# Kernel optimization log

Hardware: AMD Instinct MI355X
Metric: run time of the kernel (lower is better)

Reference implementation:

```python
import jax, jax.numpy as jnp
import numpy as np

B, L, HID = 2, 2048, 2048
NH, NKV, HD = 16, 4, 128
LAT = 512
Q_PER_KV = NH // NKV
SCALE = HD ** -0.5
ROPE_THETA = 10000.0


def setup_inputs() -> dict:
    key = jax.random.key(0)
    ks = jax.random.split(key, 6)
    s = lambda fan_in: 1.0 / np.sqrt(fan_in)
    return {
        "x": jax.random.normal(ks[0], (B, L, HID), dtype=jnp.float32),
        "Wq": jax.random.normal(ks[1], (HID, NH * HD), dtype=jnp.float32) * s(HID),
        "Wc": jax.random.normal(ks[2], (HID, LAT), dtype=jnp.float32) * s(HID),
        "Wk": jax.random.normal(ks[3], (LAT, NKV * HD), dtype=jnp.float32) * s(LAT),
        "Wv": jax.random.normal(ks[4], (LAT, NKV * HD), dtype=jnp.float32) * s(LAT),
        "Wo": jax.random.normal(ks[5], (NH * HD, HID), dtype=jnp.float32) * s(NH * HD),
        "attention_mask": jnp.ones((B, L), dtype=jnp.int32),
    }


def _rope(t):  # t: [B, H, L, HD]
    half = HD // 2
    inv_freq = 1.0 / (ROPE_THETA ** (jnp.arange(half, dtype=jnp.float32) / half))
    pos = jnp.arange(t.shape[2], dtype=jnp.float32)
    freqs = pos[:, None] * inv_freq[None, :]          # [L, half]
    cos = jnp.cos(freqs)[None, None].astype(t.dtype)  # [1,1,L,half]
    sin = jnp.sin(freqs)[None, None].astype(t.dtype)
    t1, t2 = t[..., :half], t[..., half:]
    return jnp.concatenate([t1 * cos - t2 * sin, t2 * cos + t1 * sin], axis=-1)


def reference(x, Wq, Wc, Wk, Wv, Wo, attention_mask):
    q = (x @ Wq).reshape(B, L, NH, HD).transpose(0, 2, 1, 3)      # [B,NH,L,HD]
    c = x @ Wc                                                    # latent bottleneck
    k = (c @ Wk).reshape(B, L, NKV, HD).transpose(0, 2, 1, 3)     # [B,NKV,L,HD]
    v = (c @ Wv).reshape(B, L, NKV, HD).transpose(0, 2, 1, 3)
    # GQA repeat_interleave along head axis
    k = jnp.repeat(k, Q_PER_KV, axis=1)                           # [B,NH,L,HD]
    v = jnp.repeat(v, Q_PER_KV, axis=1)
    q = _rope(q)
    k = _rope(k)
    att = jnp.einsum("bhqd,bhkd->bhqk", q, k) * SCALE             # [B,NH,L,L]
    neg = jnp.finfo(att.dtype).min
    causal = jnp.tril(jnp.ones((L, L), dtype=bool))[None, None]
    att = jnp.where(causal, att, neg)
    key_mask = (attention_mask > 0)[:, None, None, :]             # [B,1,1,L]
    att = jnp.where(key_mask, att, neg)
    att = jax.nn.softmax(att, axis=-1)
    y = jnp.einsum("bhqk,bhkd->bhqd", att, v)
    y = y.transpose(0, 2, 1, 3).reshape(B, L, NH * HD)
    return y @ Wo
```

## Files before the change

kernel.cpp:

```cpp
#include <hip/hip_runtime.h>
#include <hip/hip_bf16.h>
#include <cstdint>
#include <cstddef>

#define B_    2
#define L_    2048
#define HID_  2048
#define NH_   16
#define NKV_  4
#define HD_   128
#define LAT_  512
#define SCALE_ 0.08838834764831845f
#define SC2_   0.1275174365f

typedef unsigned short u16;
typedef unsigned int   u32;
typedef __attribute__((ext_vector_type(8))) short   short8;
typedef __attribute__((ext_vector_type(4))) float   floatx4;

typedef __attribute__((address_space(1))) const u32 gas_u32;
typedef __attribute__((address_space(3))) u32       las_u32;

__device__ __forceinline__ void gl_lds16(const u16* g, u16* l) {
    __builtin_amdgcn_global_load_lds((gas_u32*)g, (las_u32*)l, 16, 0, 0);
}

__device__ __forceinline__ float bf2f(u16 u) {
    union { u32 i; float f; } v; v.i = ((u32)u) << 16; return v.f;
}
__device__ __forceinline__ u16 f2bf(float f) {
    union { float f; u32 u; } v; v.f = f;
    u32 u = v.u;
    u32 r = (u + 0x7fffu + ((u >> 16) & 1u)) >> 16;
    return (u16)r;
}
__device__ __forceinline__ u16 f2bf_hw(float f) {
    union { __hip_bfloat16 h; u16 u; } c;
    c.h = __float2bfloat16(f);
    return c.u;
}

__global__ void cvt_kernel(const float* __restrict__ in, u16* __restrict__ out, int n4) {
    int i = blockIdx.x * 256 + threadIdx.x;
    if (i < n4) {
        float4 v = ((const float4*)in)[i];
        union { u16 w[4]; uint2 v; } o;
        o.w[0] = f2bf(v.x); o.w[1] = f2bf(v.y);
        o.w[2] = f2bf(v.z); o.w[3] = f2bf(v.w);
        ((uint2*)out)[i] = o.v;
    }
}

__global__ void cvt_transpose_kernel(const float* __restrict__ in, u16* __restrict__ out,
                                     int R, int C) {
    __shared__ u16 tile[32][33];
    int c0 = blockIdx.x * 32, r0 = blockIdx.y * 32;
    int tx = threadIdx.x & 31, ty = threadIdx.x >> 5;
    for (int i = ty; i < 32; i += 8)
        tile[tx][i] = f2bf(in[(size_t)(r0 + i) * C + c0 + tx]);
    __syncthreads();
    for (int i = ty; i < 32; i += 8)
        out[(size_t)(c0 + i) * R + r0 + tx] = tile[i][tx];
}

__global__ void transpose_v_kernel(const u16* __restrict__ in, u16* __restrict__ out) {
    __shared__ u16 t[32][33];
    int lt = blockIdx.x, dt = blockIdx.y, bh = blockIdx.z;
    int b = bh >> 2, kvh = bh & 3;
    int tx = threadIdx.x & 31, ty = threadIdx.x >> 5;
    for (int i = ty; i < 32; i += 8)
        t[i][tx] = in[(((size_t)b * L_ + lt * 32 + i) * NKV_ + kvh) * HD_ + dt * 32 + tx];
    __syncthreads();
    const int lcol = lt * 32 + tx;
    const int csig = (lcol & ~63) | ((lcol & 15) << 2) | ((lcol >> 4) & 3);
    for (int i = ty; i < 32; i += 8)
        out[((size_t)bh * HD_ + dt * 32 + i) * L_ + csig] = t[tx][i];
}

template<int OUT_BF16>
__global__ __launch_bounds__(256)
void gemm_bt(const u16* __restrict__ A, const u16* __restrict__ BT,
             void* __restrict__ C, int M, int N, int K) {
    __shared__ __align__(16) u16 As[128][32];
    __shared__ __align__(16) u16 Bs[128][32];
    const int tid  = threadIdx.x;
    const int m0   = blockIdx.y * 128, n0 = blockIdx.x * 128;
    const int wave = tid >> 6, lane = tid & 63;
    const int wm   = (wave >> 1) * 64, wn = (wave & 1) * 64;
    const int quad = lane >> 4, l16 = lane & 15;

    const int srow = wave * 32 + (lane >> 2);
    const int scol = (lane & 3) * 8;
    const u16* aptr0 = A  + (size_t)(m0 + srow) * K + scol;
    const u16* bptr0 = BT + (size_t)(n0 + srow) * K + scol;
    const u16* aptr1 = aptr0 + (size_t)16 * K;
    const u16* bptr1 = bptr0 + (size_t)16 * K;
    u16* lA0 = &As[wave * 32][0];
    u16* lA1 = &As[wave * 32 + 16][0];
    u16* lB0 = &Bs[wave * 32][0];
    u16* lB1 = &Bs[wave * 32 + 16][0];

    floatx4 acc[4][4] = {};

    for (int k0 = 0; k0 < K; k0 += 32) {
        gl_lds16(aptr0 + k0, lA0);
        gl_lds16(aptr1 + k0, lA1);
        gl_lds16(bptr0 + k0, lB0);
        gl_lds16(bptr1 + k0, lB1);
        __syncthreads();

        short8 af[4], bfr[4];
        #pragma unroll
        for (int i = 0; i < 4; i++) af[i]  = *(const short8*)&As[wm + i * 16 + l16][quad * 8];
        #pragma unroll
        for (int i = 0; i < 4; i++) bfr[i] = *(const short8*)&Bs[wn + i * 16 + l16][quad * 8];
        #pragma unroll
        for (int mi = 0; mi < 4; mi++)
            #pragma unroll
            for (int ni = 0; ni < 4; ni++)
                acc[mi][ni] = __builtin_amdgcn_mfma_f32_16x16x32_bf16(
                    af[mi], bfr[ni], acc[mi][ni], 0, 0, 0);
        __syncthreads();
    }

    #pragma unroll
    for (int mi = 0; mi < 4; mi++) {
        #pragma unroll
        for (int ni = 0; ni < 4; ni++) {
            #pragma unroll
            for (int r = 0; r < 4; r++) {
                int row = m0 + wm + mi * 16 + quad * 4 + r;
                int col = n0 + wn + ni * 16 + l16;
                float v = acc[mi][ni][r];
                if (OUT_BF16) ((u16*)C)[(size_t)row * N + col] = f2bf(v);
                else          ((float*)C)[(size_t)row * N + col] = v;
            }
        }
    }
}

__global__ __launch_bounds__(256)
void gemm_bt_split(const u16* __restrict__ A, const u16* __restrict__ BT,
                   u16* __restrict__ C0, u16* __restrict__ C1,
                   int M, int N, int K, int Nsplit, int N0, int N1) {
    __shared__ __align__(16) u16 As[128][32];
    __shared__ __align__(16) u16 Bs[128][32];
    const int tid  = threadIdx.x;
    const int m0   = blockIdx.y * 128, n0 = blockIdx.x * 128;
    const int wave = tid >> 6, lane = tid & 63;
    const int wm   = (wave >> 1) * 64, wn = (wave & 1) * 64;
    const int quad = lane >> 4, l16 = lane & 15;

    const int srow = wave * 32 + (lane >> 2);
    const int scol = (lane & 3) * 8;
    const u16* aptr0 = A  + (size_t)(m0 + srow) * K + scol;
    const u16* bptr0 = BT + (size_t)(n0 + srow) * K + scol;
    const u16* aptr1 = aptr0 + (size_t)16 * K;
    const u16* bptr1 = bptr0 + (size_t)16 * K;
    u16* lA0 = &As[wave * 32][0];
    u16* lA1 = &As[wave * 32 + 16][0];
    u16* lB0 = &Bs[wave * 32][0];
    u16* lB1 = &Bs[wave * 32 + 16][0];

    floatx4 acc[4][4] = {};

    for (int k0 = 0; k0 < K; k0 += 32) {
        gl_lds16(aptr0 + k0, lA0);
        gl_lds16(aptr1 + k0, lA1);
        gl_lds16(bptr0 + k0, lB0);
        gl_lds16(bptr1 + k0, lB1);
        __syncthreads();

        short8 af[4], bfr[4];
        #pragma unroll
        for (int i = 0; i < 4; i++) af[i]  = *(const short8*)&As[wm + i * 16 + l16][quad * 8];
        #pragma unroll
        for (int i = 0; i < 4; i++) bfr[i] = *(const short8*)&Bs[wn + i * 16 + l16][quad * 8];
        #pragma unroll
        for (int mi = 0; mi < 4; mi++)
            #pragma unroll
            for (int ni = 0; ni < 4; ni++)
                acc[mi][ni] = __builtin_amdgcn_mfma_f32_16x16x32_bf16(
                    af[mi], bfr[ni], acc[mi][ni], 0, 0, 0);
        __syncthreads();
    }

    const int side = (n0 >= Nsplit);
    u16* Cw = side ? C1 : C0;
    const int nw = side ? N1 : N0;
    const int cbase = side ? Nsplit : 0;

    #pragma unroll
    for (int mi = 0; mi < 4; mi++) {
        #pragma unroll
        for (int ni = 0; ni < 4; ni++) {
            #pragma unroll
            for (int r = 0; r < 4; r++) {
                int row = m0 + wm + mi * 16 + quad * 4 + r;
                int col = n0 + wn + ni * 16 + l16 - cbase;
                Cw[(size_t)row * nw + col] = f2bf(acc[mi][ni][r]);
            }
        }
    }
}

__global__ void rope_perm(const u16* __restrict__ in, u16* __restrict__ out,
                          int nh, int nhbits) {
    int idx = blockIdx.x * 256 + threadIdx.x;
    int d = idx & 63;
    int l = (idx >> 6) & (L_ - 1);
    int h = (idx >> 17) & (nh - 1);
    int b = idx >> (17 + nhbits);
    const u16* src = &in[(((size_t)b * L_ + l) * nh + h) * HD_];
    u16* dst = &out[(((size_t)b * nh + h) * L_ + l) * HD_];
    float t1 = bf2f(src[d]), t2 = bf2f(src[d + 64]);
    float inv = expf(-(float)d * 0.14391156831212787f);
    float fr = (float)l * inv;
    float c = cosf(fr), sn = sinf(fr);
    dst[d]      = f2bf(t1 * c - t2 * sn);
    dst[d + 64] = f2bf(t2 * c + t1 * sn);
}

__global__ __launch_bounds__(256)
void attn_mfma(const u16* __restrict__ Q, const u16* __restrict__ K,
               const u16* __restrict__ Vt, const int* __restrict__ amask,
               u16* __restrict__ Y, float* __restrict__ Opart,
               float* __restrict__ lpart) {
    __shared__ __align__(16) u16 Ks[64][128];
    __shared__ __align__(16) u16 Vs[128][64];
    __shared__ int smask[64];

    const int tid  = threadIdx.x;
    const int wave = tid >> 6, lane = tid & 63;
    const int quad = lane >> 4, l16 = lane & 15;

    const int bid = blockIdx.x;
    const int s   = bid >> 8;
    const int c   = bid & 255;
    const int bkvh = c & 7;
    const int j   = c >> 3;
    const int b   = bkvh >> 2, kvh = bkvh & 3;

    const int H  = ((32 + j) >> 1) + 1;
    const int Lg = ((31 - j) >> 1) + 1;
    const int m2 = max((H + 1) >> 1, (Lg + 1) >> 1);
    const int m3 = max((H + 2) / 3, Lg);
    const int nh = (m2 <= m3) ? 2 : 3;
    const int nl = 4 - nh;
    int t, kt0, kt1, pi;
    if (s < nh) {
        t = 32 + j; kt0 = (H * s) / nh; kt1 = (H * (s + 1)) / nh; pi = bid;
    } else {
        t = 31 - j;
        const int ls = s - nh;
        kt0 = (Lg * ls) / nl; kt1 = (Lg * (ls + 1)) / nl;
        pi = (nl == 1) ? -1 : bid;
    }

    const int h   = kvh * 4 + wave;
    const int q0  = t * 32;

    const u16* Qbase = Q  + ((size_t)b * NH_  + h)   * L_ * HD_;
    const u16* Kbase = K  + ((size_t)b * NKV_ + kvh) * L_ * HD_;
    const u16* Vbase = Vt + ((size_t)b * NKV_ + kvh) * (size_t)HD_ * L_;
    const int* mbase = amask + b * L_;

    short8 qa[2][4];
    #pragma unroll
    for (int mi = 0; mi < 2; ++mi)
        #pragma unroll
        for (int ks = 0; ks < 4; ++ks)
            qa[mi][ks] = *(const short8*)&Qbase[(size_t)(q0 + mi * 16 + l16) * HD_ + ks * 32 + quad * 8];

    floatx4 Oacc[2][8] = {};
    float lsum[2][4] = {};

    const int krow = tid >> 2, kq0 = (tid & 3) * 4;
    const int vrow = tid >> 1, vc0 = (tid & 1) * 4;
    const int kr7  = krow & 7, vr7 = vrow & 7;
    u16* kdst0 = &Ks[krow][((kq0 + 0) ^ kr7) * 8];
    u16* kdst1 = &Ks[krow][((kq0 + 1) ^ kr7) * 8];
    u16* kdst2 = &Ks[krow][((kq0 + 2) ^ kr7) * 8];
    u16* kdst3 = &Ks[krow][((kq0 + 3) ^ kr7) * 8];
    u16* vdst0 = &Vs[vrow][((vc0 + 0) ^ vr7) * 8];
    u16* vdst1 = &Vs[vrow][((vc0 + 1) ^ vr7) * 8];
    u16* vdst2 = &Vs[vrow][((vc0 + 2) ^ vr7) * 8];
    u16* vdst3 = &Vs[vrow][((vc0 + 3) ^ vr7) * 8];
    const u16* ksrc = Kbase + ((size_t)(kt0 * 64 + krow)) * HD_ + kq0 * 8;
    const u16* vsrc = Vbase + (size_t)vrow * L_ + kt0 * 64 + vc0 * 8;

    u16* Psb = &Ks[0][0] + wave * 2048;

    for (int kt = kt0; kt < kt1; ++kt) {
        const int kbase = kt * 64;

        *(uint4*)kdst0 = *(const uint4*)(ksrc);
        *(uint4*)kdst1 = *(const uint4*)(ksrc + 8);
        *(uint4*)kdst2 = *(const uint4*)(ksrc + 16);
        *(uint4*)kdst3 = *(const uint4*)(ksrc + 24);
        *(uint4*)vdst0 = *(const uint4*)(vsrc);
        *(uint4*)vdst1 = *(const uint4*)(vsrc + 8);
        *(uint4*)vdst2 = *(const uint4*)(vsrc + 16);
        *(uint4*)vdst3 = *(const uint4*)(vsrc + 24);
        if (tid < 64) smask[tid] = mbase[kbase + tid];
        ksrc += (size_t)64 * HD_;
        vsrc += 64;
        __syncthreads();

        floatx4 sfr[2][4] = {};
        __builtin_amdgcn_s_setprio(1);
        #pragma unroll
        for (int ni = 0; ni < 4; ++ni) {
            #pragma unroll
            for (int ks = 0; ks < 4; ++ks) {
                short8 kf = *(const short8*)&Ks[ni * 16 + l16][((ks * 4 + quad) ^ (l16 & 7)) * 8];
                sfr[0][ni] = __builtin_amdgcn_mfma_f32_16x16x32_bf16(qa[0][ks], kf, sfr[0][ni], 0, 0, 0);
                sfr[1][ni] = __builtin_amdgcn_mfma_f32_16x16x32_bf16(qa[1][ks], kf, sfr[1][ni], 0, 0, 0);
            }
        }
        __builtin_amdgcn_s_setprio(0);

        int am[4];
        #pragma unroll
        for (int ni = 0; ni < 4; ++ni) am[ni] = smask[ni * 16 + l16];

        __syncthreads();

        #pragma unroll
        for (int mi = 0; mi < 2; ++mi) {
            #pragma unroll
            for (int r = 0; r < 4; ++r) {
                const int qrow = q0 + mi * 16 + quad * 4 + r;
                union { u16 w[4]; uint2 v; } pb;
                #pragma unroll
                for (int ni = 0; ni < 4; ++ni) {
                    const int kpos = kbase + ni * 16 + l16;
                    const bool ok = (kpos <= qrow) & (am[ni] > 0);
                    float p = ok ? exp2f(fmaf(sfr[mi][ni][r], SC2_, -8.0f)) : 0.0f;
                    lsum[mi][r] += p;
                    pb.w[ni] = f2bf_hw(p);
                }
                const int row = mi * 16 + quad * 4 + r;
                *(uint2*)&Psb[row * 64 + ((l16 ^ ((row & 7) << 1)) << 2)] = pb.v;
            }
        }

        short8 pf[2][2];
        #pragma unroll
        for (int mi = 0; mi < 2; ++mi)
            #pragma unroll
            for (int kc = 0; kc < 2; ++kc) {
                const int row = mi * 16 + l16;
                const int p0 = (kc * 8 + quad * 2) ^ ((l16 & 7) << 1);
                pf[mi][kc] = *(const short8*)&Psb[row * 64 + p0 * 4];
            }

        __builtin_amdgcn_s_setprio(1);
        #pragma unroll
        for (int kc = 0; kc < 2; ++kc) {
            #pragma unroll
            for (int dn = 0; dn < 8; ++dn) {
                short8 vf = *(const short8*)&Vs[dn * 16 + l16][((kc * 4 + quad) ^ (l16 & 7)) * 8];
                Oacc[0][dn] = __builtin_amdgcn_mfma_f32_16x16x32_bf16(pf[0][kc], vf, Oacc[0][dn], 0, 0, 0);
                Oacc[1][dn] = __builtin_amdgcn_mfma_f32_16x16x32_bf16(pf[1][kc], vf, Oacc[1][dn], 0, 0, 0);
            }
        }
        __builtin_amdgcn_s_setprio(0);
        __syncthreads();
    }

    if (pi < 0) {
        #pragma unroll
        for (int mi = 0; mi < 2; ++mi) {
            #pragma unroll
            for (int r = 0; r < 4; ++r) {
                float v = lsum[mi][r];
                v += __shfl_xor(v, 1);
                v += __shfl_xor(v, 2);
                v += __shfl_xor(v, 4);
                v += __shfl_xor(v, 8);
                const float linv = 1.0f / v;
                const int qrow = q0 + mi * 16 + quad * 4 + r;
                u16* dst = &Y[(((size_t)b * L_ + qrow) * NH_ + h) * HD_];
                #pragma unroll
                for (int dn = 0; dn < 8; ++dn)
                    dst[dn * 16 + l16] = f2bf(Oacc[mi][dn][r] * linv);
            }
        }
    } else {
        float* od = Opart + ((size_t)pi * 4 + wave) * 32 * 128;
        float* lp = lpart + ((size_t)pi * 4 + wave) * 32;
        #pragma unroll
        for (int mi = 0; mi < 2; ++mi) {
            #pragma unroll
            for (int r = 0; r < 4; ++r) {
                float v = lsum[mi][r];
                v += __shfl_xor(v, 1);
                v += __shfl_xor(v, 2);
                v += __shfl_xor(v, 4);
                v += __shfl_xor(v, 8);
                const int qi = mi * 16 + quad * 4 + r;
                if (l16 == 0) __builtin_nontemporal_store(v, &lp[qi]);
                #pragma unroll
                for (int dn = 0; dn < 8; ++dn)
                    __builtin_nontemporal_store(Oacc[mi][dn][r],
                                                &od[(size_t)qi * 128 + dn * 16 + l16]);
            }
        }
    }
}

__global__ __launch_bounds__(256)
void attn_combine(const float* __restrict__ Opart, const float* __restrict__ lpart,
                  u16* __restrict__ Y) {
    const int cb = blockIdx.x;
    const int c  = cb & 255, z = cb >> 8;
    const int tile = z >> 2, hw = z & 3;
    const int bkvh = c & 7, j = c >> 3;
    const int b = bkvh >> 2, kvh = bkvh & 3;
    const int h = kvh * 4 + hw;
    const int H  = ((32 + j) >> 1) + 1;
    const int Lg = ((31 - j) >> 1) + 1;
    const int m2 = max((H + 1) >> 1, (Lg + 1) >> 1);
    const int m3 = max((H + 2) / 3, Lg);
    const int nh = (m2 <= m3) ? 2 : 3;
    const int nl = 4 - nh;
    if (tile == 1 && nl == 1) return;
    const int s0 = tile ? nh : 0;
    const int ns = tile ? nl : nh;
    const int t  = tile ? (31 - j) : (32 + j);
    const int tid = threadIdx.x;
    const int q = tid >> 3, dg = tid & 7;

    float4 a0 = {0,0,0,0}, a1 = {0,0,0,0}, a2 = {0,0,0,0}, a3 = {0,0,0,0};
    float lacc = 0.0f;
    for (int i = 0; i < ns; ++i) {
        const size_t rowb = ((size_t)((s0 + i) * 256 + c) * 4 + hw) * 32 + q;
        lacc += lpart[rowb];
        const float4* op = (const float4*)(Opart + rowb * 128 + dg * 16);
        float4 v0 = op[0], v1 = op[1], v2 = op[2], v3 = op[3];
        a0.x += v0.x; a0.y += v0.y; a0.z += v0.z; a0.w += v0.w;
        a1.x += v1.x; a1.y += v1.y; a1.z += v1.z; a1.w += v1.w;
        a2.x += v2.x; a2.y += v2.y; a2.z += v2.z; a2.w += v2.w;
        a3.x += v3.x; a3.y += v3.y; a3.z += v3.z; a3.w += v3.w;
    }
    const float linv = 1.0f / lacc;
    const int qrow = t * 32 + q;
    u16* dst = &Y[(((size_t)b * L_ + qrow) * NH_ + h) * HD_ + dg * 16];

    u16 tmp[16];
    tmp[0]  = f2bf(a0.x * linv); tmp[1]  = f2bf(a0.y * linv);
    tmp[2]  = f2bf(a0.z * linv); tmp[3]  = f2bf(a0.w * linv);
    tmp[4]  = f2bf(a1.x * linv); tmp[5]  = f2bf(a1.y * linv);
    tmp[6]  = f2bf(a1.z * linv); tmp[7]  = f2bf(a1.w * linv);
    tmp[8]  = f2bf(a2.x * linv); tmp[9]  = f2bf(a2.y * linv);
    tmp[10] = f2bf(a2.z * linv); tmp[11] = f2bf(a2.w * linv);
    tmp[12] = f2bf(a3.x * linv); tmp[13] = f2bf(a3.y * linv);
    tmp[14] = f2bf(a3.z * linv); tmp[15] = f2bf(a3.w * linv);
    *(uint4*)(dst)     = *(const uint4*)(&tmp[0]);
    *(uint4*)(dst + 8) = *(const uint4*)(&tmp[8]);
}

extern "C" void kernel_launch(void* const* d_in, const int* in_sizes, int n_in,
                              void* d_out, int out_size, void* d_ws, size_t ws_size,
                              hipStream_t stream) {
    const float* x  = (const float*)d_in[0];
    const float* Wq = (const float*)d_in[1];
    const float* Wc = (const float*)d_in[2];
    const float* Wk = (const float*)d_in[3];
    const float* Wv = (const float*)d_in[4];
    const float* Wo = (const float*)d_in[5];
    const int* amask = (const int*)d_in[6];
    float* out = (float*)d_out;

    char* p = (char*)d_ws;
    auto alloc = [&](size_t elems) {
        u16* r = (u16*)p;
        p += ((elems * 2 + 255) / 256) * 256;
        return r;
    };
    u16* WoT  = alloc((size_t)2048 * 2048);
    u16* qbuf = alloc((size_t)4096 * 2048);
    u16* Qr   = alloc((size_t)4096 * 2048);
    u16* Kr   = alloc((size_t)4096 * 512);
    u16* Vt   = alloc((size_t)4096 * 512);
    char* pdead = p;
    u16* Xb   = alloc((size_t)4096 * 2048);
    u16* WqT  = alloc((size_t)2048 * 2048);
    u16* WcT  = alloc((size_t)512 * 2048);
    u16* WkT  = alloc((size_t)512 * 512);
    u16* WvT  = alloc((size_t)512 * 512);
    u16* cbuf = alloc((size_t)4096 * 512);
    u16* kbuf = alloc((size_t)4096 * 512);
    u16* vbuf = alloc((size_t)4096 * 512);
    float* Opart = (float*)pdead;
    float* lpart = (float*)(pdead + (size_t)1024 * 4 * 32 * 128 * 4);

    cvt_kernel<<<8388608 / 4 / 256, 256, 0, stream>>>(x, Xb, 8388608 / 4);
    cvt_transpose_kernel<<<dim3(2048 / 32, 2048 / 32), 256, 0, stream>>>(Wq, WqT, 2048, 2048);
    cvt_transpose_kernel<<<dim3(512 / 32, 2048 / 32), 256, 0, stream>>>(Wc, WcT, 2048, 512);
    cvt_transpose_kernel<<<dim3(512 / 32, 512 / 32), 256, 0, stream>>>(Wk, WkT, 512, 512);
    cvt_transpose_kernel<<<dim3(512 / 32, 512 / 32), 256, 0, stream>>>(Wv, WvT, 512, 512);
    cvt_transpose_kernel<<<dim3(2048 / 32, 2048 / 32), 256, 0, stream>>>(Wo, WoT, 2048, 2048);

    gemm_bt_split<<<dim3(20, 32), 256, 0, stream>>>(Xb, WqT, qbuf, cbuf,
                                                    4096, 2560, 2048, 2048, 2048, 512);
    gemm_bt_split<<<dim3(8, 32), 256, 0, stream>>>(cbuf, WkT, kbuf, vbuf,
                                                   4096, 1024, 512, 512, 512, 512);

    rope_perm<<<(2 * 16 * 2048 * 64) / 256, 256, 0, stream>>>(qbuf, Qr, 16, 4);
    rope_perm<<<(2 * 4 * 2048 * 64) / 256, 256, 0, stream>>>(kbuf, Kr, 4, 2);
    transpose_v_kernel<<<dim3(64, 4, 8), 256, 0, stream>>>(vbuf, Vt);

    attn_mfma<<<dim3(1024), 256, 0, stream>>>(Qr, Kr, Vt, amask, qbuf, Opart, lpart);
    attn_combine<<<dim3(2048), 256, 0, stream>>>(Opart, lpart, qbuf);

    gemm_bt<0><<<dim3(16, 32), 256, 0, stream>>>(qbuf, WoT, out, 4096, 2048, 2048);
}
```

Before: 374.2 us.

## Keep attention probabilities in registers via transposed QK MFMA and direct LDS loads

The QK^T MFMA swaps its operands so each lane holds scores in the layout the PV MFMA needs. This removes the LDS round-trip for P and one __syncthreads per key tile, and the V transpose permutation is changed to match. K/V tiles are loaded with global_load_lds instead of register staging. A fast path skips masking when the tile is fully below the diagonal and the attention mask is all ones. Row sums are reduced with fewer shuffles. The risk is getting the layout permutation wrong and adding extra per-tile mask loads from global memory.

```diff
diff --git a/kernel.cpp b/kernel.cpp
--- a/kernel.cpp
+++ b/kernel.cpp
@@ -72,7 +72,10 @@
         t[i][tx] = in[(((size_t)b * L_ + lt * 32 + i) * NKV_ + kvh) * HD_ + dt * 32 + tx];
     __syncthreads();
     const int lcol = lt * 32 + tx;
-    const int csig = (lcol & ~63) | ((lcol & 15) << 2) | ((lcol >> 4) & 3);
+    const int k6 = lcol & 63;
+    const int ni = k6 >> 4, qd = (k6 >> 2) & 3, r = k6 & 3;
+    const int p = ((ni >> 1) << 5) | (qd << 3) | ((ni & 1) << 2) | r;
+    const int csig = (lcol & ~63) | p;
     for (int i = ty; i < 32; i += 8)
         out[((size_t)bh * HD_ + dt * 32 + i) * L_ + csig] = t[tx][i];
 }
@@ -228,7 +231,6 @@
                float* __restrict__ lpart) {
     __shared__ __align__(16) u16 Ks[64][128];
     __shared__ __align__(16) u16 Vs[128][64];
-    __shared__ int smask[64];
 
     const int tid  = threadIdx.x;
     const int wave = tid >> 6, lane = tid & 63;
@@ -273,38 +275,37 @@
             qa[mi][ks] = *(const short8*)&Qbase[(size_t)(q0 + mi * 16 + l16) * HD_ + ks * 32 + quad * 8];
 
     floatx4 Oacc[2][8] = {};
-    float lsum[2][4] = {};
-
-    const int krow = tid >> 2, kq0 = (tid & 3) * 4;
-    const int vrow = tid >> 1, vc0 = (tid & 1) * 4;
-    const int kr7  = krow & 7, vr7 = vrow & 7;
-    u16* kdst0 = &Ks[krow][((kq0 + 0) ^ kr7) * 8];
-    u16* kdst1 = &Ks[krow][((kq0 + 1) ^ kr7) * 8];
-    u16* kdst2 = &Ks[krow][((kq0 + 2) ^ kr7) * 8];
-    u16* kdst3 = &Ks[krow][((kq0 + 3) ^ kr7) * 8];
-    u16* vdst0 = &Vs[vrow][((vc0 + 0) ^ vr7) * 8];
-    u16* vdst1 = &Vs[vrow][((vc0 + 1) ^ vr7) * 8];
-    u16* vdst2 = &Vs[vrow][((vc0 + 2) ^ vr7) * 8];
-    u16* vdst3 = &Vs[vrow][((vc0 + 3) ^ vr7) * 8];
-    const u16* ksrc = Kbase + ((size_t)(kt0 * 64 + krow)) * HD_ + kq0 * 8;
-    const u16* vsrc = Vbase + (size_t)vrow * L_ + kt0 * 64 + vc0 * 8;
-
-    u16* Psb = &Ks[0][0] + wave * 2048;
+    float lsum[2] = {0.0f, 0.0f};
+
+    const int slK = lane & 15, rKl = lane >> 4;
+    const int slV = lane & 7,  rVl = lane >> 3;
+    int okg[4], ovg[4];
+    u16 *klds[4], *vlds[4];
+    #pragma unroll
+    for (int cc = 0; cc < 4; ++cc) {
+        const int seg = wave * 4 + cc;
+        const int rk = seg * 4 + rKl;
+        okg[cc] = rk * HD_ + ((slK ^ (rk & 7)) * 8);
+        klds[cc] = (u16*)Ks + seg * 512;
+        const int rv = seg * 8 + rVl;
+        ovg[cc] = rv * L_ + ((slV ^ (rv & 7)) * 8);
+        vlds[cc] = (u16*)Vs + seg * 512;
+    }
+    const u16* kgb = Kbase + (size_t)kt0 * 64 * HD_;
+    const u16* vgb = Vbase + kt0 * 64;
 
     for (int kt = kt0; kt < kt1; ++kt) {
         const int kbase = kt * 64;
 
-        *(uint4*)kdst0 = *(const uint4*)(ksrc);
-        *(uint4*)kdst1 = *(const uint4*)(ksrc + 8);
-        *(uint4*)kdst2 = *(const uint4*)(ksrc + 16);
-        *(uint4*)kdst3 = *(const uint4*)(ksrc + 24);
-        *(uint4*)vdst0 = *(const uint4*)(vsrc);
-        *(uint4*)vdst1 = *(const uint4*)(vsrc + 8);
-        *(uint4*)vdst2 = *(const uint4*)(vsrc + 16);
-        *(uint4*)vdst3 = *(const uint4*)(vsrc + 24);
-        if (tid < 64) smask[tid] = mbase[kbase + tid];
-        ksrc += (size_t)64 * HD_;
-        vsrc += 64;
+        #pragma unroll
+        for (int cc = 0; cc < 4; ++cc) {
+            gl_lds16(kgb + okg[cc], klds[cc]);
+            gl_lds16(vgb + ovg[cc], vlds[cc]);
+        }
+        const int am_l = mbase[kbase + lane];
+        const bool allm = __all(am_l > 0);
+        kgb += (size_t)64 * HD_;
+        vgb += 64;
         __syncthreads();
 
         floatx4 sfr[2][4] = {};
@@ -314,34 +315,40 @@
             #pragma unroll
             for (int ks = 0; ks < 4; ++ks) {
                 short8 kf = *(const short8*)&Ks[ni * 16 + l16][((ks * 4 + quad) ^ (l16 & 7)) * 8];
-                sfr[0][ni] = __builtin_amdgcn_mfma_f32_16x16x32_bf16(qa[0][ks], kf, sfr[0][ni], 0, 0, 0);
-                sfr[1][ni] = __builtin_amdgcn_mfma_f32_16x16x32_bf16(qa[1][ks], kf, sfr[1][ni], 0, 0, 0);
+                sfr[0][ni] = __builtin_amdgcn_mfma_f32_16x16x32_bf16(kf, qa[0][ks], sfr[0][ni], 0, 0, 0);
+                sfr[1][ni] = __builtin_amdgcn_mfma_f32_16x16x32_bf16(kf, qa[1][ks], sfr[1][ni], 0, 0, 0);
             }
         }
         __builtin_amdgcn_s_setprio(0);
 
-        int am[4];
-        #pragma unroll
-        for (int ni = 0; ni < 4; ++ni) am[ni] = smask[ni * 16 + l16];
-
-        __syncthreads();
-
-        #pragma unroll
-        for (int mi = 0; mi < 2; ++mi) {
-            #pragma unroll
-            for (int r = 0; r < 4; ++r) {
-                const int qrow = q0 + mi * 16 + quad * 4 + r;
-                union { u16 w[4]; uint2 v; } pb;
+        if (allm & (kbase + 63 <= q0)) {
+            #pragma unroll
+            for (int mi = 0; mi < 2; ++mi)
                 #pragma unroll
-                for (int ni = 0; ni < 4; ++ni) {
-                    const int kpos = kbase + ni * 16 + l16;
-                    const bool ok = (kpos <= qrow) & (am[ni] > 0);
-                    float p = ok ? exp2f(fmaf(sfr[mi][ni][r], SC2_, -8.0f)) : 0.0f;
-                    lsum[mi][r] += p;
-                    pb.w[ni] = f2bf_hw(p);
+                for (int ni = 0; ni < 4; ++ni)
+                    #pragma unroll
+                    for (int r = 0; r < 4; ++r) {
+                        float p = exp2f(fmaf(sfr[mi][ni][r], SC2_, -8.0f));
+                        lsum[mi] += p;
+                        sfr[mi][ni][r] = p;
+                    }
+        } else {
+            #pragma unroll
+            for (int ni = 0; ni < 4; ++ni) {
+                const int4 amv = *(const int4*)&mbase[kbase + ni * 16 + quad * 4];
+                const int amr[4] = {amv.x, amv.y, amv.z, amv.w};
+                #pragma unroll
+                for (int mi = 0; mi < 2; ++mi) {
+                    const int qrow = q0 + mi * 16 + l16;
+                    #pragma unroll
+                    for (int r = 0; r < 4; ++r) {
+                        const int kpos = kbase + ni * 16 + quad * 4 + r;
+                        const bool ok = (kpos <= qrow) & (amr[r] > 0);
+                        float p = ok ? exp2f(fmaf(sfr[mi][ni][r], SC2_, -8.0f)) : 0.0f;
+                        lsum[mi] += p;
+                        sfr[mi][ni][r] = p;
+                    }
                 }
-                const int row = mi * 16 + quad * 4 + r;
-                *(uint2*)&Psb[row * 64 + ((l16 ^ ((row & 7) << 1)) << 2)] = pb.v;
             }
         }
 
@@ -350,9 +357,13 @@
         for (int mi = 0; mi < 2; ++mi)
             #pragma unroll
             for (int kc = 0; kc < 2; ++kc) {
-                const int row = mi * 16 + l16;
-                const int p0 = (kc * 8 + quad * 2) ^ ((l16 & 7) << 1);
-                pf[mi][kc] = *(const short8*)&Psb[row * 64 + p0 * 4];
+                union { u16 w[8]; short8 s8; } u;
+                #pragma unroll
+                for (int r = 0; r < 4; ++r) {
+                    u.w[r]     = f2bf_hw(sfr[mi][kc * 2][r]);
+                    u.w[4 + r] = f2bf_hw(sfr[mi][kc * 2 + 1][r]);
+                }
+                pf[mi][kc] = u.s8;
             }
 
         __builtin_amdgcn_s_setprio(1);
@@ -369,17 +380,21 @@
         __syncthreads();
     }
 
+    float lr[2];
+    #pragma unroll
+    for (int mi = 0; mi < 2; ++mi) {
+        float v = lsum[mi];
+        v += __shfl_xor(v, 16);
+        v += __shfl_xor(v, 32);
+        lr[mi] = v;
+    }
+
     if (pi < 0) {
         #pragma unroll
         for (int mi = 0; mi < 2; ++mi) {
             #pragma unroll
             for (int r = 0; r < 4; ++r) {
-                float v = lsum[mi][r];
-                v += __shfl_xor(v, 1);
-                v += __shfl_xor(v, 2);
-                v += __shfl_xor(v, 4);
-                v += __shfl_xor(v, 8);
-                const float linv = 1.0f / v;
+                const float linv = 1.0f / __shfl(lr[mi], quad * 4 + r);
                 const int qrow = q0 + mi * 16 + quad * 4 + r;
                 u16* dst = &Y[(((size_t)b * L_ + qrow) * NH_ + h) * HD_];
                 #pragma unroll
@@ -392,15 +407,11 @@
         float* lp = lpart + ((size_t)pi * 4 + wave) * 32;
         #pragma unroll
         for (int mi = 0; mi < 2; ++mi) {
+            if (quad == 0)
+                __builtin_nontemporal_store(lr[mi], &lp[mi * 16 + l16]);
             #pragma unroll
             for (int r = 0; r < 4; ++r) {
-                float v = lsum[mi][r];
-                v += __shfl_xor(v, 1);
-                v += __shfl_xor(v, 2);
-                v += __shfl_xor(v, 4);
-                v += __shfl_xor(v, 8);
                 const int qi = mi * 16 + quad * 4 + r;
-                if (l16 == 0) __builtin_nontemporal_store(v, &lp[qi]);
                 #pragma unroll
                 for (int dn = 0; dn < 8; ++dn)
                     __builtin_nontemporal_store(Oacc[mi][dn][r],
```

New measurement: 359.5 us. 1.04x faster.
